# Performance work log

Measured on AMD Instinct MI355X. Metric: run time of the kernel, lower is better.

The kernel has to match this reference:

```python
import math
import jax, jax.numpy as jnp
import numpy as np

B, T, D, H, FACTOR = 8, 4096, 1024, 16, 5
DH = D // H


def setup_inputs() -> dict:
    key = jax.random.key(0)
    ks = jax.random.split(key, 7)
    u = max(1, min(int(FACTOR * math.log(T + 1)), T))  # = 41
    s = 1.0 / np.sqrt(D).astype(np.float32)
    x = jax.random.normal(ks[0], (B, T, D), jnp.float32)
    Wq = jax.random.normal(ks[1], (D, D), jnp.float32) * s
    Wk = jax.random.normal(ks[2], (D, D), jnp.float32) * s
    Wv = jax.random.normal(ks[3], (D, D), jnp.float32) * s
    Wo = jax.random.normal(ks[4], (D, D), jnp.float32) * s
    bo = jax.random.normal(ks[5], (D,), jnp.float32) * 0.01
    # unique indices, mirroring torch.randperm(T)[:u]
    idx = jax.random.permutation(ks[6], T)[:u].astype(jnp.int32)
    return {"x": x, "Wq": Wq, "Wk": Wk, "Wv": Wv, "Wo": Wo, "bo": bo, "idx": idx}


def reference(x, Wq, Wk, Wv, Wo, bo, idx):
    Bx, Tx, Dx = x.shape
    scale = 1.0 / np.sqrt(DH).astype(np.float32)

    def proj(W):  # torch Linear: x @ W.T, then split heads -> [B,H,T,Dh]
        return (x @ W.T).reshape(Bx, Tx, H, DH).transpose(0, 2, 1, 3)

    Q = proj(Wq)
    K = proj(Wk)
    V = proj(Wv)

    Qs = Q[:, :, idx, :]                                   # [B,H,u,Dh] gather
    scores = jnp.einsum('bhud,bhtd->bhut', Qs, K) * scale  # [B,H,u,T]
    attn = jax.nn.softmax(scores, axis=-1)
    ctx = jnp.einsum('bhut,bhtd->bhud', attn, V)           # [B,H,u,Dh]

    # mean over the u sampled positions fills non-sampled slots
    out = jnp.broadcast_to(ctx.mean(axis=2, keepdims=True), (Bx, H, Tx, DH))
    out = out.at[:, :, idx, :].set(ctx)                    # scatter ctx back

    y = out.transpose(0, 2, 1, 3).reshape(Bx, Tx, Dx)
    return y @ Wo.T + bo
```

## Files before the change

### kernel.cpp

```cpp
#include <hip/hip_runtime.h>
#include <hip/hip_bf16.h>

#define B_  8
#define T_  4096
#define D_  1024
#define H_  16
#define DH_ 64

typedef __bf16 bf8 __attribute__((ext_vector_type(8)));
typedef float f32x4 __attribute__((ext_vector_type(4)));

__device__ __forceinline__ unsigned short f2bf_rn(float f) {
    unsigned u = __float_as_uint(f);
    unsigned r = (u + 0x7FFF + ((u >> 16) & 1)) >> 16;
    return (unsigned short)r;
}

__device__ __forceinline__ void async_load16(const void* gp, void* lp) {
    __builtin_amdgcn_global_load_lds(
        (const __attribute__((address_space(1))) unsigned*)(gp),
        (__attribute__((address_space(3))) unsigned*)(lp), 16, 0, 0);
}

__global__ void k_prep(const float* __restrict__ x, short* __restrict__ xb,
                       const float* __restrict__ Wv, short* __restrict__ Wvb,
                       short* __restrict__ Qtb, const int* __restrict__ idx,
                       int* __restrict__ sel, int U, int HU, int MP, int nzp) {
    int g = blockIdx.x;
    int tid = threadIdx.x;
    if (g < 16896) {
        const float* src = (g < 16384) ? x : Wv;
        short* dst = (g < 16384) ? xb : Wvb;
        size_t gg = (g < 16384) ? g : (g - 16384);
        size_t i = (gg * 256 + tid) * 8;
        float4 a = *(const float4*)(src + i);
        float4 b = *(const float4*)(src + i + 4);
        short4 s0, s1;
        s0.x = (short)f2bf_rn(a.x); s0.y = (short)f2bf_rn(a.y);
        s0.z = (short)f2bf_rn(a.z); s0.w = (short)f2bf_rn(a.w);
        s1.x = (short)f2bf_rn(b.x); s1.y = (short)f2bf_rn(b.y);
        s1.z = (short)f2bf_rn(b.z); s1.w = (short)f2bf_rn(b.w);
        *(short4*)(dst + i) = s0;
        *(short4*)(dst + i + 4) = s1;
    } else if (g < 16896 + nzp) {
        int bi = g - 16896;
        int npad = MP - HU;
        int b = bi / npad, r = bi - b * npad;
        short4 z = {0, 0, 0, 0};
        *(short4*)(Qtb + ((size_t)b * MP + HU + r) * D_ + tid * 4) = z;
    } else {
        for (int t = tid; t < T_; t += 256) sel[t] = 0;
        __syncthreads();
        if (tid < U) sel[idx[tid]] = tid + 1;
    }
}

__global__ __launch_bounds__(256) void k_projg(const float* __restrict__ x,
                                               const int* __restrict__ idx,
                                               const float* __restrict__ W,
                                               float* __restrict__ C, int U) {
    __shared__ float As[32][64 + 4];
    __shared__ float Bs[32][64 + 4];
    __shared__ int sidx[64];
    int M = B_ * U;
    if (threadIdx.x < U) sidx[threadIdx.x] = idx[threadIdx.x];
    __syncthreads();
    int m0 = blockIdx.x * 64, n0 = blockIdx.y * 64;
    int tid = threadIdx.x;
    int lr = tid >> 3, lc = (tid & 7) * 4;
    int ty = tid >> 4, tx = tid & 15;
    float acc[4][4] = {{0.f}};
    for (int k0 = 0; k0 < D_; k0 += 32) {
#pragma unroll
        for (int half = 0; half < 2; ++half) {
            int r = lr + half * 32;
            int gm = m0 + r;
            float4 v = make_float4(0.f, 0.f, 0.f, 0.f);
            if (gm < M) {
                int b = gm / U, i = gm - b * U;
                v = *(const float4*)(x + ((size_t)(b * T_ + sidx[i])) * D_ + k0 + lc);
            }
            As[lc + 0][r] = v.x; As[lc + 1][r] = v.y; As[lc + 2][r] = v.z; As[lc + 3][r] = v.w;
            int gn = n0 + r;
            float4 w = *(const float4*)(W + (size_t)gn * D_ + k0 + lc);
            Bs[lc + 0][r] = w.x; Bs[lc + 1][r] = w.y; Bs[lc + 2][r] = w.z; Bs[lc + 3][r] = w.w;
        }
        __syncthreads();
#pragma unroll
        for (int kk = 0; kk < 32; ++kk) {
            float4 a = *(const float4*)&As[kk][ty * 4];
            float4 bb = *(const float4*)&Bs[kk][tx * 4];
            acc[0][0] += a.x * bb.x; acc[0][1] += a.x * bb.y; acc[0][2] += a.x * bb.z; acc[0][3] += a.x * bb.w;
            acc[1][0] += a.y * bb.x; acc[1][1] += a.y * bb.y; acc[1][2] += a.y * bb.z; acc[1][3] += a.y * bb.w;
            acc[2][0] += a.z * bb.x; acc[2][1] += a.z * bb.y; acc[2][2] += a.z * bb.z; acc[2][3] += a.z * bb.w;
            acc[3][0] += a.w * bb.x; acc[3][1] += a.w * bb.y; acc[3][2] += a.w * bb.z; acc[3][3] += a.w * bb.w;
        }
        __syncthreads();
    }
#pragma unroll
    for (int i = 0; i < 4; ++i) {
        int gm = m0 + ty * 4 + i;
        if (gm < M)
            *(float4*)(C + (size_t)gm * D_ + n0 + tx * 4) =
                make_float4(acc[i][0], acc[i][1], acc[i][2], acc[i][3]);
    }
}

__global__ __launch_bounds__(256) void k_proj(const float* __restrict__ A,
                                              const float* __restrict__ W,
                                              const float* __restrict__ bias,
                                              float* __restrict__ C, int M) {
    __shared__ float As[32][64 + 4];
    __shared__ float Bs[32][64 + 4];
    int m0 = blockIdx.x * 64, n0 = blockIdx.y * 64;
    int tid = threadIdx.x;
    int lr = tid >> 3, lc = (tid & 7) * 4;
    int ty = tid >> 4, tx = tid & 15;
    float acc[4][4] = {{0.f}};
    for (int k0 = 0; k0 < D_; k0 += 32) {
#pragma unroll
        for (int half = 0; half < 2; ++half) {
            int r = lr + half * 32;
            int gm = m0 + r;
            float4 v = make_float4(0.f, 0.f, 0.f, 0.f);
            if (gm < M) v = *(const float4*)(A + (size_t)gm * D_ + k0 + lc);
            As[lc + 0][r] = v.x; As[lc + 1][r] = v.y; As[lc + 2][r] = v.z; As[lc + 3][r] = v.w;
            int gn = n0 + r;
            float4 w = *(const float4*)(W + (size_t)gn * D_ + k0 + lc);
            Bs[lc + 0][r] = w.x; Bs[lc + 1][r] = w.y; Bs[lc + 2][r] = w.z; Bs[lc + 3][r] = w.w;
        }
        __syncthreads();
#pragma unroll
        for (int kk = 0; kk < 32; ++kk) {
            float4 a = *(const float4*)&As[kk][ty * 4];
            float4 bb = *(const float4*)&Bs[kk][tx * 4];
            acc[0][0] += a.x * bb.x; acc[0][1] += a.x * bb.y; acc[0][2] += a.x * bb.z; acc[0][3] += a.x * bb.w;
            acc[1][0] += a.y * bb.x; acc[1][1] += a.y * bb.y; acc[1][2] += a.y * bb.z; acc[1][3] += a.y * bb.w;
            acc[2][0] += a.z * bb.x; acc[2][1] += a.z * bb.y; acc[2][2] += a.z * bb.z; acc[2][3] += a.z * bb.w;
            acc[3][0] += a.w * bb.x; acc[3][1] += a.w * bb.y; acc[3][2] += a.w * bb.z; acc[3][3] += a.w * bb.w;
        }
        __syncthreads();
    }
#pragma unroll
    for (int i = 0; i < 4; ++i) {
        int gm = m0 + ty * 4 + i;
        if (gm < M) {
            int gn = n0 + tx * 4;
            float4 v = make_float4(acc[i][0], acc[i][1], acc[i][2], acc[i][3]);
            if (bias) {
                v.x += bias[gn + 0]; v.y += bias[gn + 1];
                v.z += bias[gn + 2]; v.w += bias[gn + 3];
            }
            *(float4*)(C + (size_t)gm * D_ + gn) = v;
        }
    }
}

__global__ __launch_bounds__(256) void k_qth(const float* __restrict__ Qs,
                                             const float* __restrict__ Wk,
                                             short* __restrict__ Qtb, int U, int MP) {
    __shared__ float As[32][64 + 4];
    __shared__ float Bs[32][64 + 4];
    int h = blockIdx.z;
    int m0 = blockIdx.x * 64, n0 = blockIdx.y * 64;
    int BU = B_ * U;
    int tid = threadIdx.x;
    int lr = tid >> 3, lc = (tid & 7) * 4;
    int ty = tid >> 4, tx = tid & 15;
    float acc[4][4] = {{0.f}};
    for (int k0 = 0; k0 < DH_; k0 += 32) {
#pragma unroll
        for (int half = 0; half < 2; ++half) {
            int r = lr + half * 32;
            int gm = m0 + r;
            float4 v = make_float4(0.f, 0.f, 0.f, 0.f);
            if (gm < BU) v = *(const float4*)(Qs + (size_t)gm * D_ + h * DH_ + k0 + lc);
            As[lc + 0][r] = v.x; As[lc + 1][r] = v.y; As[lc + 2][r] = v.z; As[lc + 3][r] = v.w;
            int kr = (tid >> 4) + half * 16;
            int nc = (tid & 15) * 4;
            float4 w = *(const float4*)(Wk + ((size_t)(h * DH_ + k0 + kr)) * D_ + n0 + nc);
            *(float4*)&Bs[kr][nc] = w;
        }
        __syncthreads();
#pragma unroll
        for (int kk = 0; kk < 32; ++kk) {
            float4 a = *(const float4*)&As[kk][ty * 4];
            float4 bb = *(const float4*)&Bs[kk][tx * 4];
            acc[0][0] += a.x * bb.x; acc[0][1] += a.x * bb.y; acc[0][2] += a.x * bb.z; acc[0][3] += a.x * bb.w;
            acc[1][0] += a.y * bb.x; acc[1][1] += a.y * bb.y; acc[1][2] += a.y * bb.z; acc[1][3] += a.y * bb.w;
            acc[2][0] += a.z * bb.x; acc[2][1] += a.z * bb.y; acc[2][2] += a.z * bb.z; acc[2][3] += a.z * bb.w;
            acc[3][0] += a.w * bb.x; acc[3][1] += a.w * bb.y; acc[3][2] += a.w * bb.z; acc[3][3] += a.w * bb.w;
        }
        __syncthreads();
    }
#pragma unroll
    for (int i = 0; i < 4; ++i) {
        int gm = m0 + ty * 4 + i;
        if (gm < BU) {
            int b = gm / U, ii = gm - b * U;
            short4 s;
            s.x = (short)f2bf_rn(0.125f * acc[i][0]);
            s.y = (short)f2bf_rn(0.125f * acc[i][1]);
            s.z = (short)f2bf_rn(0.125f * acc[i][2]);
            s.w = (short)f2bf_rn(0.125f * acc[i][3]);
            *(short4*)(Qtb + ((size_t)b * MP + h * U + ii) * D_ + n0 + tx * 4) = s;
        }
    }
}

__global__ __launch_bounds__(256) void k_scores_v(const short* __restrict__ Qtb,
                                                  const short* __restrict__ xb,
                                                  const short* __restrict__ Wvb,
                                                  short* __restrict__ attnb,
                                                  short* __restrict__ Vt, int MP) {
    __shared__ short smem[8192];
    short* As = smem;
    short* Bs = smem + 4096;
    int g = blockIdx.x;
    int tid = threadIdx.x;
    int lane = tid & 63, w = tid >> 6;
    int wr = w >> 1, wc = w & 1;
    int quad = lane >> 4, l15 = lane & 15;
    const int K = D_;

    f32x4 acc[4][4];
#pragma unroll
    for (int mi = 0; mi < 4; ++mi)
#pragma unroll
        for (int ni = 0; ni < 4; ++ni)
            acc[mi][ni] = (f32x4){0.f, 0.f, 0.f, 0.f};

    int arow = wr * 64 + l15;
    int brow = wc * 64 + l15;
    int koff = quad * 8;

    if (g < 2048) {
        int b = g & 7;
        int n = (g >> 3) & 7;
        int mq = g >> 6;
        const short* Ab = xb + (size_t)(b * 32 + mq) * 128 * K;
        const short* Bb = Wvb + (size_t)n * 128 * K;
        for (int kt = 0; kt < K; kt += 32) {
#pragma unroll
            for (int i = 0; i < 2; ++i) {
                int li = i * 256 + tid;
                int row = li >> 2, kc = (li & 3) << 3;
                async_load16(Ab + (size_t)row * K + kt + kc, As + li * 8);
                async_load16(Bb + (size_t)row * K + kt + kc, Bs + li * 8);
            }
            __syncthreads();
            bf8 af[4], bfr[4];
#pragma unroll
            for (int mi = 0; mi < 4; ++mi)
                af[mi] = *(const bf8*)(As + (arow + mi * 16) * 32 + koff);
#pragma unroll
            for (int ni = 0; ni < 4; ++ni)
                bfr[ni] = *(const bf8*)(Bs + (brow + ni * 16) * 32 + koff);
#pragma unroll
            for (int mi = 0; mi < 4; ++mi)
#pragma unroll
                for (int ni = 0; ni < 4; ++ni)
                    acc[mi][ni] = __builtin_amdgcn_mfma_f32_16x16x32_bf16(af[mi], bfr[ni], acc[mi][ni], 0, 0, 0);
            __syncthreads();
        }
        int tG0 = mq * 128 + wr * 64;
        int h = n * 2 + wc;
        short* ep = smem + w * 2048;
        const int PITCH = 72;
#pragma unroll
        for (int ni = 0; ni < 4; ++ni) {
#pragma unroll
            for (int mi = 0; mi < 4; ++mi) {
                short4 s;
                s.x = (short)f2bf_rn(acc[mi][ni][0]);
                s.y = (short)f2bf_rn(acc[mi][ni][1]);
                s.z = (short)f2bf_rn(acc[mi][ni][2]);
                s.w = (short)f2bf_rn(acc[mi][ni][3]);
                *(short4*)(ep + l15 * PITCH + mi * 16 + quad * 4) = s;
            }
#pragma unroll
            for (int it = 0; it < 2; ++it) {
                int dhl = it * 8 + (lane >> 3);
                int seg = lane & 7;
                bf8 v = *(const bf8*)(ep + dhl * PITCH + seg * 8);
                int dh = ni * 16 + dhl;
                *(bf8*)(Vt + ((size_t)(b * H_ + h) * DH_ + dh) * T_ + tG0 + seg * 8) = v;
            }
        }
    } else {
        int gs = g - 2048;
        int b = gs & 7;
        int r2 = gs >> 3;
        int m = r2 % 6;
        int n = r2 / 6;
        const short* Ab = Qtb + (size_t)b * MP * K;
        const short* Bb = xb + (size_t)b * T_ * K;
        short* Cb = attnb + (size_t)b * MP * T_;
        int m0 = m * 128, n0 = n * 128;
        for (int kt = 0; kt < K; kt += 32) {
#pragma unroll
            for (int i = 0; i < 2; ++i) {
                int li = i * 256 + tid;
                int row = li >> 2, kc = (li & 3) << 3;
                async_load16(Ab + (size_t)(m0 + row) * K + kt + kc, As + li * 8);
                async_load16(Bb + (size_t)(n0 + row) * K + kt + kc, Bs + li * 8);
            }
            __syncthreads();
            bf8 af[4], bfr[4];
#pragma unroll
            for (int mi = 0; mi < 4; ++mi)
                af[mi] = *(const bf8*)(As + (arow + mi * 16) * 32 + koff);
#pragma unroll
            for (int ni = 0; ni < 4; ++ni)
                bfr[ni] = *(const bf8*)(Bs + (brow + ni * 16) * 32 + koff);
#pragma unroll
            for (int ni = 0; ni < 4; ++ni)
#pragma unroll
                for (int mi = 0; mi < 4; ++mi)
                    acc[ni][mi] = __builtin_amdgcn_mfma_f32_16x16x32_bf16(bfr[ni], af[mi], acc[ni][mi], 0, 0, 0);
            __syncthreads();
        }
#pragma unroll
        for (int ni = 0; ni < 4; ++ni)
#pragma unroll
            for (int mi = 0; mi < 4; ++mi) {
                int grow = m0 + wr * 64 + mi * 16 + l15;
                int col = n0 + wc * 64 + ni * 16 + quad * 4;
                short4 s;
                s.x = (short)f2bf_rn(__expf(acc[ni][mi][0]));
                s.y = (short)f2bf_rn(__expf(acc[ni][mi][1]));
                s.z = (short)f2bf_rn(__expf(acc[ni][mi][2]));
                s.w = (short)f2bf_rn(__expf(acc[ni][mi][3]));
                *(short4*)(Cb + (size_t)grow * T_ + col) = s;
            }
    }
}

#define VPITCH 136
__global__ __launch_bounds__(256) void k_pvT(const short* __restrict__ attnb,
                                             const short* __restrict__ Vt,
                                             float* __restrict__ R, int U, int MP) {
    __shared__ short sm[(64 + 48) * VPITCH];
    __shared__ float redbuf[64 * 48];
    __shared__ float inv[48];
    short* vs = sm;
    short* ps = sm + 64 * VPITCH;
    int gid = blockIdx.x;
    int h = gid & (H_ - 1), b = gid >> 4;
    int tid = threadIdx.x, lane = tid & 63, w = tid >> 6;
    int l15 = lane & 15, quad = lane >> 4;
    const short* Pg = attnb + ((size_t)b * MP + h * U) * T_;
    const short* Vg = Vt + ((size_t)(b * H_ + h)) * DH_ * T_;

    f32x4 acc[4][3];
#pragma unroll
    for (int mf = 0; mf < 4; ++mf)
#pragma unroll
        for (int nf = 0; nf < 3; ++nf)
            acc[mf][nf] = (f32x4){0.f, 0.f, 0.f, 0.f};
    float rspart = 0.f;

    int vrow = tid >> 2, vseg = tid & 3;

    for (int kt = 0; kt < T_; kt += 128) {
        {
            const short* src = Vg + (size_t)vrow * T_ + kt + vseg * 32;
            short* d = vs + vrow * VPITCH + vseg * 32;
            bf8 v0 = *(const bf8*)(src);
            bf8 v1 = *(const bf8*)(src + 8);
            bf8 v2 = *(const bf8*)(src + 16);
            bf8 v3 = *(const bf8*)(src + 24);
            *(bf8*)(d) = v0; *(bf8*)(d + 8) = v1; *(bf8*)(d + 16) = v2; *(bf8*)(d + 24) = v3;
        }
        if (tid < 192) {
            const short* src = Pg + (size_t)vrow * T_ + kt + vseg * 32;
            short* d = ps + vrow * VPITCH + vseg * 32;
            bf8 v0 = *(const bf8*)(src);
            bf8 v1 = *(const bf8*)(src + 8);
            bf8 v2 = *(const bf8*)(src + 16);
            bf8 v3 = *(const bf8*)(src + 24);
            *(bf8*)(d) = v0; *(bf8*)(d + 8) = v1; *(bf8*)(d + 16) = v2; *(bf8*)(d + 24) = v3;
#pragma unroll
            for (int j = 0; j < 8; ++j)
                rspart += (float)v0[j] + (float)v1[j] + (float)v2[j] + (float)v3[j];
        }
        __syncthreads();
        bf8 af[4], bfr[3];
#pragma unroll
        for (int mf = 0; mf < 4; ++mf)
            af[mf] = *(const bf8*)(vs + (mf * 16 + l15) * VPITCH + w * 32 + quad * 8);
#pragma unroll
        for (int nf = 0; nf < 3; ++nf)
            bfr[nf] = *(const bf8*)(ps + (nf * 16 + l15) * VPITCH + w * 32 + quad * 8);
#pragma unroll
        for (int mf = 0; mf < 4; ++mf)
#pragma unroll
            for (int nf = 0; nf < 3; ++nf)
                acc[mf][nf] = __builtin_amdgcn_mfma_f32_16x16x32_bf16(af[mf], bfr[nf], acc[mf][nf], 0, 0, 0);
        __syncthreads();
    }

    for (int wv = 0; wv < 4; ++wv) {
        if (w == wv) {
#pragma unroll
            for (int mf = 0; mf < 4; ++mf)
#pragma unroll
                for (int nf = 0; nf < 3; ++nf)
#pragma unroll
                    for (int r = 0; r < 4; ++r) {
                        int i2 = (mf * 16 + quad * 4 + r) * 48 + nf * 16 + l15;
                        if (wv == 0) redbuf[i2] = acc[mf][nf][r];
                        else redbuf[i2] += acc[mf][nf][r];
                    }
        }
        __syncthreads();
    }
    float* rsf = (float*)sm;
    if (tid < 192) rsf[tid] = rspart;
    __syncthreads();
    if (tid < 48)
        inv[tid] = 1.f / (rsf[tid * 4] + rsf[tid * 4 + 1] + rsf[tid * 4 + 2] + rsf[tid * 4 + 3]);
    __syncthreads();
    int dh = tid >> 2, part = tid & 3;
    float msum = 0.f;
#pragma unroll
    for (int j = 0; j < 12; ++j) {
        int q = part * 12 + j;
        if (q < U) {
            float v = redbuf[dh * 48 + q] * inv[q];
            R[((size_t)b * (U + 1) + 1 + q) * D_ + h * DH_ + dh] = v;
            msum += v;
        }
    }
    msum += __shfl_down(msum, 1);
    msum += __shfl_down(msum, 2);
    if (part == 0)
        R[((size_t)b * (U + 1)) * D_ + h * DH_ + dh] = msum / (float)U;
}

__global__ __launch_bounds__(256) void k_fill(const float* __restrict__ Yr,
                                              const int* __restrict__ sel,
                                              float* __restrict__ y, int U) {
    int blk = blockIdx.x;
    int b = blk >> 12, t = blk & (T_ - 1);
    int j = sel[t];
    const float4* src = (const float4*)(Yr + ((size_t)b * (U + 1) + j) * D_);
    float4* dst = (float4*)(y + (size_t)blk * D_);
    dst[threadIdx.x] = src[threadIdx.x];
}

extern "C" void kernel_launch(void* const* d_in, const int* in_sizes, int n_in,
                              void* d_out, int out_size, void* d_ws, size_t ws_size,
                              hipStream_t stream) {
    const float* x  = (const float*)d_in[0];
    const float* Wq = (const float*)d_in[1];
    const float* Wk = (const float*)d_in[2];
    const float* Wv = (const float*)d_in[3];
    const float* Wo = (const float*)d_in[4];
    const float* bo = (const float*)d_in[5];
    const int*  idx = (const int*)d_in[6];
    int U = in_sizes[6];
    int HU = H_ * U;
    int MP = ((HU + 127) / 128) * 128;
    int nzp = B_ * (MP - HU);

    char* w = (char*)d_ws;
    auto alloc = [&](size_t bytes) { char* p = w; w += (bytes + 255) & ~(size_t)255; return p; };

    float* Qs    = (float*)alloc((size_t)B_ * U * D_ * 4);
    short* Qtb   = (short*)alloc((size_t)B_ * MP * D_ * 2);
    short* xb    = (short*)alloc((size_t)B_ * T_ * D_ * 2);
    short* Wvb   = (short*)alloc((size_t)D_ * D_ * 2);
    short* attnb = (short*)alloc((size_t)B_ * MP * T_ * 2);
    short* Vtb   = (short*)alloc((size_t)B_ * D_ * T_ * 2);
    float* R     = (float*)alloc((size_t)B_ * (U + 1) * D_ * 4);
    float* Yr    = (float*)alloc((size_t)B_ * (U + 1) * D_ * 4);
    int*   sel   = (int*)alloc((size_t)T_ * 4);

    k_prep<<<dim3(16896 + nzp + 1), dim3(256), 0, stream>>>(x, xb, Wv, Wvb, Qtb, idx, sel, U, HU, MP, nzp);
    k_projg<<<dim3((B_ * U + 63) / 64, D_ / 64), dim3(256), 0, stream>>>(x, idx, Wq, Qs, U);
    k_qth<<<dim3((B_ * U + 63) / 64, D_ / 64, H_), dim3(256), 0, stream>>>(Qs, Wk, Qtb, U, MP);
    k_scores_v<<<dim3(2048 + 1536), dim3(256), 0, stream>>>(Qtb, xb, Wvb, attnb, Vtb, MP);
    k_pvT<<<dim3(B_ * H_), dim3(256), 0, stream>>>(attnb, Vtb, R, U, MP);
    k_proj<<<dim3((B_ * (U + 1) + 63) / 64, D_ / 64), dim3(256), 0, stream>>>(R, Wo, bo, Yr, B_ * (U + 1));
    k_fill<<<dim3(B_ * T_), dim3(256), 0, stream>>>(Yr, sel, (float*)d_out, U);
}
```

Baseline: 593.6 us.

## Split PV over T chunks with reduction kernel; double K-step in GEMM loop

The PV kernel previously ran only 128 blocks, one per batch-head, looping over all T. It now splits T into 4 chunks, giving 512 blocks, and writes partial outputs and row sums. A new small kernel reduces those partials, normalises, and computes the mean row. Each wave now owns 16 dh rows, which removes the in-block cross-wave reduction. Separately, the scores/V GEMM loads two 32-wide K slices per barrier pair, halving the synchronisations at the cost of twice the LDS. The trade-offs are an extra launch, extra global traffic for the partials, and possibly lower occupancy from the larger LDS footprint.

```diff
diff --git a/kernel.cpp b/kernel.cpp
--- a/kernel.cpp
+++ b/kernel.cpp
@@ -6,6 +6,7 @@
 #define D_  1024
 #define H_  16
 #define DH_ 64
+#define NC_ 4
 
 typedef __bf16 bf8 __attribute__((ext_vector_type(8)));
 typedef float f32x4 __attribute__((ext_vector_type(4)));
@@ -213,9 +214,9 @@
                                                   const short* __restrict__ Wvb,
                                                   short* __restrict__ attnb,
                                                   short* __restrict__ Vt, int MP) {
-    __shared__ short smem[8192];
-    short* As = smem;
-    short* Bs = smem + 4096;
+    __shared__ short smem[16384];
+    short* Abuf[2] = { smem, smem + 4096 };
+    short* Bbuf[2] = { smem + 8192, smem + 12288 };
     int g = blockIdx.x;
     int tid = threadIdx.x;
     int lane = tid & 63, w = tid >> 6;
@@ -240,27 +241,32 @@
         int mq = g >> 6;
         const short* Ab = xb + (size_t)(b * 32 + mq) * 128 * K;
         const short* Bb = Wvb + (size_t)n * 128 * K;
-        for (int kt = 0; kt < K; kt += 32) {
-#pragma unroll
-            for (int i = 0; i < 2; ++i) {
-                int li = i * 256 + tid;
-                int row = li >> 2, kc = (li & 3) << 3;
-                async_load16(Ab + (size_t)row * K + kt + kc, As + li * 8);
-                async_load16(Bb + (size_t)row * K + kt + kc, Bs + li * 8);
-            }
+        for (int kt = 0; kt < K; kt += 64) {
+#pragma unroll
+            for (int hb = 0; hb < 2; ++hb)
+#pragma unroll
+                for (int i = 0; i < 2; ++i) {
+                    int li = i * 256 + tid;
+                    int row = li >> 2, kc = (li & 3) << 3;
+                    async_load16(Ab + (size_t)row * K + kt + hb * 32 + kc, Abuf[hb] + li * 8);
+                    async_load16(Bb + (size_t)row * K + kt + hb * 32 + kc, Bbuf[hb] + li * 8);
+                }
             __syncthreads();
-            bf8 af[4], bfr[4];
-#pragma unroll
-            for (int mi = 0; mi < 4; ++mi)
-                af[mi] = *(const bf8*)(As + (arow + mi * 16) * 32 + koff);
-#pragma unroll
-            for (int ni = 0; ni < 4; ++ni)
-                bfr[ni] = *(const bf8*)(Bs + (brow + ni * 16) * 32 + koff);
-#pragma unroll
-            for (int mi = 0; mi < 4; ++mi)
+#pragma unroll
+            for (int hb = 0; hb < 2; ++hb) {
+                bf8 af[4], bfr[4];
+#pragma unroll
+                for (int mi = 0; mi < 4; ++mi)
+                    af[mi] = *(const bf8*)(Abuf[hb] + (arow + mi * 16) * 32 + koff);
 #pragma unroll
                 for (int ni = 0; ni < 4; ++ni)
-                    acc[mi][ni] = __builtin_amdgcn_mfma_f32_16x16x32_bf16(af[mi], bfr[ni], acc[mi][ni], 0, 0, 0);
+                    bfr[ni] = *(const bf8*)(Bbuf[hb] + (brow + ni * 16) * 32 + koff);
+#pragma unroll
+                for (int mi = 0; mi < 4; ++mi)
+#pragma unroll
+                    for (int ni = 0; ni < 4; ++ni)
+                        acc[mi][ni] = __builtin_amdgcn_mfma_f32_16x16x32_bf16(af[mi], bfr[ni], acc[mi][ni], 0, 0, 0);
+            }
             __syncthreads();
         }
         int tG0 = mq * 128 + wr * 64;
@@ -297,27 +303,32 @@
         const short* Bb = xb + (size_t)b * T_ * K;
         short* Cb = attnb + (size_t)b * MP * T_;
         int m0 = m * 128, n0 = n * 128;
-        for (int kt = 0; kt < K; kt += 32) {
-#pragma unroll
-            for (int i = 0; i < 2; ++i) {
-                int li = i * 256 + tid;
-                int row = li >> 2, kc = (li & 3) << 3;
-                async_load16(Ab + (size_t)(m0 + row) * K + kt + kc, As + li * 8);
-                async_load16(Bb + (size_t)(n0 + row) * K + kt + kc, Bs + li * 8);
-            }
+        for (int kt = 0; kt < K; kt += 64) {
+#pragma unroll
+            for (int hb = 0; hb < 2; ++hb)
+#pragma unroll
+                for (int i = 0; i < 2; ++i) {
+                    int li = i * 256 + tid;
+                    int row = li >> 2, kc = (li & 3) << 3;
+                    async_load16(Ab + (size_t)(m0 + row) * K + kt + hb * 32 + kc, Abuf[hb] + li * 8);
+                    async_load16(Bb + (size_t)(n0 + row) * K + kt + hb * 32 + kc, Bbuf[hb] + li * 8);
+                }
             __syncthreads();
-            bf8 af[4], bfr[4];
-#pragma unroll
-            for (int mi = 0; mi < 4; ++mi)
-                af[mi] = *(const bf8*)(As + (arow + mi * 16) * 32 + koff);
-#pragma unroll
-            for (int ni = 0; ni < 4; ++ni)
-                bfr[ni] = *(const bf8*)(Bs + (brow + ni * 16) * 32 + koff);
-#pragma unroll
-            for (int ni = 0; ni < 4; ++ni)
+#pragma unroll
+            for (int hb = 0; hb < 2; ++hb) {
+                bf8 af[4], bfr[4];
 #pragma unroll
                 for (int mi = 0; mi < 4; ++mi)
-                    acc[ni][mi] = __builtin_amdgcn_mfma_f32_16x16x32_bf16(bfr[ni], af[mi], acc[ni][mi], 0, 0, 0);
+                    af[mi] = *(const bf8*)(Abuf[hb] + (arow + mi * 16) * 32 + koff);
+#pragma unroll
+                for (int ni = 0; ni < 4; ++ni)
+                    bfr[ni] = *(const bf8*)(Bbuf[hb] + (brow + ni * 16) * 32 + koff);
+#pragma unroll
+                for (int ni = 0; ni < 4; ++ni)
+#pragma unroll
+                    for (int mi = 0; mi < 4; ++mi)
+                        acc[ni][mi] = __builtin_amdgcn_mfma_f32_16x16x32_bf16(bfr[ni], af[mi], acc[ni][mi], 0, 0, 0);
+            }
             __syncthreads();
         }
 #pragma unroll
@@ -339,30 +350,30 @@
 #define VPITCH 136
 __global__ __launch_bounds__(256) void k_pvT(const short* __restrict__ attnb,
                                              const short* __restrict__ Vt,
-                                             float* __restrict__ R, int U, int MP) {
+                                             float* __restrict__ Op,
+                                             float* __restrict__ rsp,
+                                             int U, int MP) {
     __shared__ short sm[(64 + 48) * VPITCH];
-    __shared__ float redbuf[64 * 48];
-    __shared__ float inv[48];
     short* vs = sm;
     short* ps = sm + 64 * VPITCH;
     int gid = blockIdx.x;
-    int h = gid & (H_ - 1), b = gid >> 4;
+    int c = gid & (NC_ - 1);
+    int bh = gid >> 2;
+    int h = bh & (H_ - 1), b = bh >> 4;
     int tid = threadIdx.x, lane = tid & 63, w = tid >> 6;
     int l15 = lane & 15, quad = lane >> 4;
     const short* Pg = attnb + ((size_t)b * MP + h * U) * T_;
     const short* Vg = Vt + ((size_t)(b * H_ + h)) * DH_ * T_;
 
-    f32x4 acc[4][3];
-#pragma unroll
-    for (int mf = 0; mf < 4; ++mf)
-#pragma unroll
-        for (int nf = 0; nf < 3; ++nf)
-            acc[mf][nf] = (f32x4){0.f, 0.f, 0.f, 0.f};
+    f32x4 acc[3];
+#pragma unroll
+    for (int nf = 0; nf < 3; ++nf) acc[nf] = (f32x4){0.f, 0.f, 0.f, 0.f};
     float rspart = 0.f;
 
     int vrow = tid >> 2, vseg = tid & 3;
 
-    for (int kt = 0; kt < T_; kt += 128) {
+    for (int tt = 0; tt < (T_ / NC_) / 128; ++tt) {
+        int kt = c * (T_ / NC_) + tt * 128;
         {
             const short* src = Vg + (size_t)vrow * T_ + kt + vseg * 32;
             short* d = vs + vrow * VPITCH + vseg * 32;
@@ -385,57 +396,62 @@
                 rspart += (float)v0[j] + (float)v1[j] + (float)v2[j] + (float)v3[j];
         }
         __syncthreads();
-        bf8 af[4], bfr[3];
-#pragma unroll
-        for (int mf = 0; mf < 4; ++mf)
-            af[mf] = *(const bf8*)(vs + (mf * 16 + l15) * VPITCH + w * 32 + quad * 8);
-#pragma unroll
-        for (int nf = 0; nf < 3; ++nf)
-            bfr[nf] = *(const bf8*)(ps + (nf * 16 + l15) * VPITCH + w * 32 + quad * 8);
-#pragma unroll
-        for (int mf = 0; mf < 4; ++mf)
-#pragma unroll
-            for (int nf = 0; nf < 3; ++nf)
-                acc[mf][nf] = __builtin_amdgcn_mfma_f32_16x16x32_bf16(af[mf], bfr[nf], acc[mf][nf], 0, 0, 0);
-        __syncthreads();
-    }
-
-    for (int wv = 0; wv < 4; ++wv) {
-        if (w == wv) {
-#pragma unroll
-            for (int mf = 0; mf < 4; ++mf)
-#pragma unroll
-                for (int nf = 0; nf < 3; ++nf)
-#pragma unroll
-                    for (int r = 0; r < 4; ++r) {
-                        int i2 = (mf * 16 + quad * 4 + r) * 48 + nf * 16 + l15;
-                        if (wv == 0) redbuf[i2] = acc[mf][nf][r];
-                        else redbuf[i2] += acc[mf][nf][r];
-                    }
-        }
-        __syncthreads();
-    }
+#pragma unroll
+        for (int kc = 0; kc < 4; ++kc) {
+            bf8 af = *(const bf8*)(vs + (w * 16 + l15) * VPITCH + kc * 32 + quad * 8);
+#pragma unroll
+            for (int nf = 0; nf < 3; ++nf) {
+                bf8 bfr = *(const bf8*)(ps + (nf * 16 + l15) * VPITCH + kc * 32 + quad * 8);
+                acc[nf] = __builtin_amdgcn_mfma_f32_16x16x32_bf16(af, bfr, acc[nf], 0, 0, 0);
+            }
+        }
+        __syncthreads();
+    }
+#pragma unroll
+    for (int nf = 0; nf < 3; ++nf)
+#pragma unroll
+        for (int r = 0; r < 4; ++r)
+            Op[((size_t)gid * 48 + nf * 16 + l15) * DH_ + w * 16 + quad * 4 + r] = acc[nf][r];
     float* rsf = (float*)sm;
     if (tid < 192) rsf[tid] = rspart;
     __syncthreads();
     if (tid < 48)
-        inv[tid] = 1.f / (rsf[tid * 4] + rsf[tid * 4 + 1] + rsf[tid * 4 + 2] + rsf[tid * 4 + 3]);
+        rsp[(size_t)gid * 48 + tid] =
+            rsf[tid * 4] + rsf[tid * 4 + 1] + rsf[tid * 4 + 2] + rsf[tid * 4 + 3];
+}
+
+__global__ __launch_bounds__(256) void k_rows2(const float* __restrict__ Op,
+                                               const float* __restrict__ rsp,
+                                               float* __restrict__ R, int U) {
+    __shared__ float inv[48];
+    __shared__ float msum[4][64];
+    int bh = blockIdx.x;
+    int b = bh >> 4, h = bh & (H_ - 1);
+    int tid = threadIdx.x;
+    if (tid < 48) {
+        float s = 0.f;
+        for (int cc = 0; cc < NC_; ++cc) s += rsp[(size_t)(bh * NC_ + cc) * 48 + tid];
+        inv[tid] = 1.f / s;
+    }
     __syncthreads();
-    int dh = tid >> 2, part = tid & 3;
-    float msum = 0.f;
-#pragma unroll
-    for (int j = 0; j < 12; ++j) {
-        int q = part * 12 + j;
-        if (q < U) {
-            float v = redbuf[dh * 48 + q] * inv[q];
-            R[((size_t)b * (U + 1) + 1 + q) * D_ + h * DH_ + dh] = v;
-            msum += v;
-        }
-    }
-    msum += __shfl_down(msum, 1);
-    msum += __shfl_down(msum, 2);
-    if (part == 0)
-        R[((size_t)b * (U + 1)) * D_ + h * DH_ + dh] = msum / (float)U;
+    int dh = tid & 63, ig = tid >> 6;
+    float acc = 0.f;
+    for (int p = 0; p < 11; ++p) {
+        int i = p * 4 + ig;
+        if (i < U) {
+            float o = 0.f;
+            for (int cc = 0; cc < NC_; ++cc)
+                o += Op[((size_t)(bh * NC_ + cc) * 48 + i) * DH_ + dh];
+            float v = o * inv[i];
+            R[((size_t)b * (U + 1) + 1 + i) * D_ + h * DH_ + dh] = v;
+            acc += v;
+        }
+    }
+    msum[ig][dh] = acc;
+    __syncthreads();
+    if (ig == 0)
+        R[((size_t)b * (U + 1)) * D_ + h * DH_ + dh] =
+            (msum[0][dh] + msum[1][dh] + msum[2][dh] + msum[3][dh]) / (float)U;
 }
 
 __global__ __launch_bounds__(256) void k_fill(const float* __restrict__ Yr,
@@ -473,6 +489,8 @@
     short* Wvb   = (short*)alloc((size_t)D_ * D_ * 2);
     short* attnb = (short*)alloc((size_t)B_ * MP * T_ * 2);
     short* Vtb   = (short*)alloc((size_t)B_ * D_ * T_ * 2);
+    float* Opb   = (float*)alloc((size_t)B_ * H_ * NC_ * 48 * DH_ * 4);
+    float* rspb  = (float*)alloc((size_t)B_ * H_ * NC_ * 48 * 4);
     float* R     = (float*)alloc((size_t)B_ * (U + 1) * D_ * 4);
     float* Yr    = (float*)alloc((size_t)B_ * (U + 1) * D_ * 4);
     int*   sel   = (int*)alloc((size_t)T_ * 4);
@@ -481,7 +499,8 @@
     k_projg<<<dim3((B_ * U + 63) / 64, D_ / 64), dim3(256), 0, stream>>>(x, idx, Wq, Qs, U);
     k_qth<<<dim3((B_ * U + 63) / 64, D_ / 64, H_), dim3(256), 0, stream>>>(Qs, Wk, Qtb, U, MP);
     k_scores_v<<<dim3(2048 + 1536), dim3(256), 0, stream>>>(Qtb, xb, Wvb, attnb, Vtb, MP);
-    k_pvT<<<dim3(B_ * H_), dim3(256), 0, stream>>>(attnb, Vtb, R, U, MP);
+    k_pvT<<<dim3(B_ * H_ * NC_), dim3(256), 0, stream>>>(attnb, Vtb, Opb, rspb, U, MP);
+    k_rows2<<<dim3(B_ * H_), dim3(256), 0, stream>>>(Opb, rspb, R, U);
     k_proj<<<dim3((B_ * (U + 1) + 63) / 64, D_ / 64), dim3(256), 0, stream>>>(R, Wo, bo, Yr, B_ * (U + 1));
     k_fill<<<dim3(B_ * T_), dim3(256), 0, stream>>>(Yr, sel, (float*)d_out, U);
 }
```

Result: no change. 596.0 us (+0.4%).
